# Performance work log

Hardware: AMD Instinct MI355X
Metric: run time of the kernel (lower is better)

## Reference

```python
import jax, jax.numpy as jnp
import numpy as np

B, A, H1, H2 = 128, 64, 256, 256


def setup_inputs() -> dict:
    key = jax.random.key(0)
    k1, k2, k3, k4, k5, k6 = jax.random.split(key, 6)
    scale = 0.01
    return {
        "userAspRep": jax.random.normal(k1, (B, A, H1), dtype=jnp.float32),
        "itemAspRep": jax.random.normal(k2, (B, A, H1), dtype=jnp.float32),
        "W_u": jax.random.uniform(k3, (H2, H1), jnp.float32, -scale, scale),
        "W_i": jax.random.uniform(k4, (H2, H1), jnp.float32, -scale, scale),
        "w_hu": jax.random.uniform(k5, (H2, 1), jnp.float32, -scale, scale),
        "w_hi": jax.random.uniform(k6, (H2, 1), jnp.float32, -scale, scale),
    }


def reference(userAspRep, itemAspRep, W_u, W_i, w_hu, w_hi):
    # L1 pairwise similarity: sim[b,u,i] = 1 / (1 + sum_h |U[b,u,h] - I[b,i,h]|)
    diff = jnp.abs(userAspRep[:, :, None, :] - itemAspRep[:, None, :, :])  # [B,Au,Ai,H1]
    sim = 1.0 / (1.0 + diff.sum(axis=-1))  # [B,Au,Ai]

    Wu_u = jnp.einsum('kh,buh->bku', W_u, userAspRep)  # [B,H2,Au]
    Wi_i = jnp.einsum('kh,bih->bki', W_i, itemAspRep)  # [B,H2,Ai]

    # User aspect importance
    H_u = jax.nn.relu(Wu_u + jnp.einsum('bki,bui->bku', Wi_i, sim))  # [B,H2,Au]
    user_scores = jnp.einsum('k,bku->bu', w_hu[:, 0], H_u)  # [B,Au]
    userAspImpt = jax.nn.softmax(user_scores, axis=1)

    # Item aspect importance
    H_i = jax.nn.relu(Wi_i + jnp.einsum('bku,bui->bki', Wu_u, sim))  # [B,H2,Ai]
    item_scores = jnp.einsum('k,bki->bi', w_hi[:, 0], H_i)  # [B,Ai]
    itemAspImpt = jax.nn.softmax(item_scores, axis=1)

    return (userAspImpt, itemAspImpt)
```

## Files before the change

kernel.cpp:

```cpp
#include <hip/hip_runtime.h>

#define NB 128
#define NA 64
#define NH1 256
#define NH2 256

typedef __attribute__((ext_vector_type(8))) short bf16x8;
typedef __attribute__((ext_vector_type(4))) float f32x4;
typedef __attribute__((ext_vector_type(8))) unsigned short u16x8;
typedef __attribute__((ext_vector_type(4))) unsigned short u16x4;
typedef _Float16 f16x2 __attribute__((ext_vector_type(2)));

__device__ __forceinline__ unsigned short f2bf(float f) {
    union { float f; unsigned u; } v; v.f = f;
    unsigned r = v.u + 0x7FFFu + ((v.u >> 16) & 1u);
    return (unsigned short)(r >> 16);
}
__device__ __forceinline__ f16x2 habs2(f16x2 x) {
    union { f16x2 h; unsigned u; } v; v.h = x; v.u &= 0x7FFF7FFFu; return v.h;
}

#define XSWZ(row, cb) ((cb) ^ (((row) & 7) << 4))

#define SROW 264
__global__ __launch_bounds__(1024) void sim_kernel(
    const float* __restrict__ U, const float* __restrict__ I,
    const float* __restrict__ Wu, const float* __restrict__ Wi,
    unsigned short* __restrict__ Wub, unsigned short* __restrict__ Wib,
    unsigned short* __restrict__ SIM, unsigned short* __restrict__ SIMT)
{
    __shared__ __align__(16) _Float16 sh[96 * SROW];
    const int t = threadIdx.x, b = blockIdx.x, uh = blockIdx.y;

    if (t < 512) {
        const int bl = b * 2 + uh;
        const int e = bl * 512 + t;
        if (e < 65536) Wub[e] = f2bf(Wu[e]);
        else           Wib[e - 65536] = f2bf(Wi[e - 65536]);
    }

    const float4* Ug = reinterpret_cast<const float4*>(U + ((size_t)b * NA + uh * 32) * NH1);
    const float4* Ig = reinterpret_cast<const float4*>(I + (size_t)b * NA * NH1);
    #pragma unroll
    for (int it = 0; it < 6; ++it) {
        const int g = t + it * 1024;
        float4 v = (g < 2048) ? Ug[g] : Ig[g - 2048];
        const int row = g >> 6, c4 = g & 63;
        f16x2 h0; h0.x = (_Float16)v.x; h0.y = (_Float16)v.y;
        f16x2 h1; h1.x = (_Float16)v.z; h1.y = (_Float16)v.w;
        union { f16x2 h[2]; float2 f; } pk; pk.h[0] = h0; pk.h[1] = h1;
        *reinterpret_cast<float2*>(&sh[row * SROW + c4 * 4]) = pk.f;
    }
    __syncthreads();

    const int tx = t & 15;
    const int hh = (t >> 4) & 1;
    const int ty = t >> 5;
    f16x2 acc[4];
    #pragma unroll
    for (int di = 0; di < 4; ++di) { acc[di].x = (_Float16)0; acc[di].y = (_Float16)0; }

    const _Float16* Urow = &sh[ty * SROW + hh * 128];
    #pragma unroll 4
    for (int h8 = 0; h8 < 16; ++h8) {
        union { float4 f; f16x2 h[4]; } uv, iv;
        uv.f = *reinterpret_cast<const float4*>(&Urow[h8 * 8]);
        #pragma unroll
        for (int di = 0; di < 4; ++di) {
            iv.f = *reinterpret_cast<const float4*>(
                &sh[(32 + tx + di * 16) * SROW + hh * 128 + h8 * 8]);
            #pragma unroll
            for (int c = 0; c < 4; ++c)
                acc[di] = acc[di] + habs2(uv.h[c] - iv.h[c]);
        }
    }

    float s[4];
    #pragma unroll
    for (int di = 0; di < 4; ++di) {
        s[di] = (float)acc[di].x + (float)acc[di].y;
        s[di] += __shfl_xor(s[di], 16, 64);
    }
    if (hh == 0) {
        const int u = uh * 32 + ty;
        unsigned short* SB = SIM  + (size_t)b * NA * NA;
        unsigned short* TB = SIMT + (size_t)b * NA * NA;
        #pragma unroll
        for (int di = 0; di < 4; ++di) {
            const int i = tx + di * 16;
            const unsigned short sv = f2bf(1.0f / (1.0f + s[di]));
            SB[(size_t)u * NA + i] = sv;
            TB[(size_t)i * NA + u] = sv;
        }
    }
}

__global__ __launch_bounds__(1024) void fused_kernel(
    const float* __restrict__ U, const float* __restrict__ I,
    const unsigned short* __restrict__ Wub, const unsigned short* __restrict__ Wib,
    const unsigned short* __restrict__ SIM, const unsigned short* __restrict__ SIMT,
    const float* __restrict__ whu, const float* __restrict__ whi,
    float* __restrict__ out)
{
    __shared__ __align__(16) unsigned short Xl[2 * 64 * 256];
    __shared__ __align__(16) unsigned short Pl[256 * 64];
    __shared__ float red[16 * 64];
    const int t = threadIdx.x, b = blockIdx.x, s = blockIdx.y;

    #pragma unroll
    for (int it = 0; it < 8; ++it) {
        const int g = t + it * 1024;
        const int side = g >> 12, rem = g & 4095;
        const int row = rem >> 6, c4 = rem & 63;
        const float* X = side ? I : U;
        float4 v = *reinterpret_cast<const float4*>(X + ((size_t)b * NA + row) * NH1 + c4 * 4);
        u16x4 o;
        o[0] = f2bf(v.x); o[1] = f2bf(v.y); o[2] = f2bf(v.z); o[3] = f2bf(v.w);
        char* dst = (char*)Xl + side * 32768 + row * 512 + XSWZ(row, c4 * 8);
        *reinterpret_cast<u16x4*>(dst) = o;
    }
    __syncthreads();

    const int w  = __builtin_amdgcn_readfirstlane(t >> 6);
    const int l  = t & 63;
    const int lr = l & 15;
    const int lk = (l >> 4) * 8;
    const int k0 = w * 16;

    const unsigned short* Ws = s ? Wib : Wub;
    const unsigned short* Wo = s ? Wub : Wib;

    f32x4 accO[4], accX[4];
    #pragma unroll
    for (int at = 0; at < 4; ++at) { accO[at] = (f32x4)(0.f); accX[at] = (f32x4)(0.f); }

    #pragma unroll
    for (int h0 = 0; h0 < NH1; h0 += 32) {
        bf16x8 as_, ao_, bs_[4], bo_[4];
        const size_t roff = (size_t)(k0 + lr) * NH1 + h0 + lk;
        as_ = *reinterpret_cast<const bf16x8*>(Ws + roff);
        ao_ = *reinterpret_cast<const bf16x8*>(Wo + roff);
        #pragma unroll
        for (int at = 0; at < 4; ++at) {
            const int row = at * 16 + lr;
            const int cb  = XSWZ(row, (h0 + lk) * 2);
            bs_[at] = *reinterpret_cast<const bf16x8*>((char*)Xl + s * 32768 + row * 512 + cb);
            bo_[at] = *reinterpret_cast<const bf16x8*>((char*)Xl + (s ^ 1) * 32768 + row * 512 + cb);
        }
        #pragma unroll
        for (int at = 0; at < 4; ++at) {
            accO[at] = __builtin_amdgcn_mfma_f32_16x16x32_bf16(as_, bs_[at], accO[at], 0, 0, 0);
            accX[at] = __builtin_amdgcn_mfma_f32_16x16x32_bf16(ao_, bo_[at], accX[at], 0, 0, 0);
        }
    }

    {
        const int kb = k0 + (l >> 4) * 4;
        #pragma unroll
        for (int at = 0; at < 4; ++at)
            #pragma unroll
            for (int r = 0; r < 4; ++r) {
                const int row = kb + r;
                *reinterpret_cast<unsigned short*>(
                    (char*)Pl + row * 128 + XSWZ(row, (at * 16 + lr) * 2)) = f2bf(accX[at][r]);
            }
    }
    __syncthreads();

    const unsigned short* SMg = (s ? SIMT : SIM) + (size_t)b * NA * NA;
    const float* wv = s ? whi : whu;

    f32x4 sacc[4];
    #pragma unroll
    for (int ot = 0; ot < 4; ++ot) sacc[ot] = (f32x4)(0.f);
    #pragma unroll
    for (int kk2 = 0; kk2 < 2; ++kk2) {
        const int arow = k0 + lr;
        bf16x8 af = *reinterpret_cast<const bf16x8*>(
            (char*)Pl + arow * 128 + XSWZ(arow, (kk2 * 32 + lk) * 2));
        #pragma unroll
        for (int ot = 0; ot < 4; ++ot) {
            bf16x8 bf = *reinterpret_cast<const bf16x8*>(
                SMg + (size_t)(ot * 16 + lr) * NA + kk2 * 32 + lk);
            sacc[ot] = __builtin_amdgcn_mfma_f32_16x16x32_bf16(af, bf, sacc[ot], 0, 0, 0);
        }
    }

    const int kb = k0 + (l >> 4) * 4;
    float wr[4];
    #pragma unroll
    for (int r = 0; r < 4; ++r) wr[r] = wv[kb + r];
    float partial[4];
    #pragma unroll
    for (int ot = 0; ot < 4; ++ot) {
        float p = 0.f;
        #pragma unroll
        for (int r = 0; r < 4; ++r) {
            float h = accO[ot][r] + sacc[ot][r];
            h = fmaxf(h, 0.f);
            p = fmaf(wr[r], h, p);
        }
        partial[ot] = p;
    }
    #pragma unroll
    for (int ot = 0; ot < 4; ++ot) {
        partial[ot] += __shfl_xor(partial[ot], 16, 64);
        partial[ot] += __shfl_xor(partial[ot], 32, 64);
    }
    if (l < 16) {
        #pragma unroll
        for (int ot = 0; ot < 4; ++ot) red[w * 64 + ot * 16 + l] = partial[ot];
    }
    __syncthreads();

    if (t < 64) {
        float sc = 0.f;
        #pragma unroll
        for (int q = 0; q < 16; ++q) sc += red[q * 64 + t];
        float m = sc;
        #pragma unroll
        for (int off = 32; off >= 1; off >>= 1) m = fmaxf(m, __shfl_xor(m, off, 64));
        float e = __expf(sc - m);
        float ssum = e;
        #pragma unroll
        for (int off = 32; off >= 1; off >>= 1) ssum += __shfl_xor(ssum, off, 64);
        out[(size_t)s * (NB * NA) + (size_t)b * NA + t] = e / ssum;
    }
}

extern "C" void kernel_launch(void* const* d_in, const int* in_sizes, int n_in,
                              void* d_out, int out_size, void* d_ws, size_t ws_size,
                              hipStream_t stream)
{
    (void)in_sizes; (void)n_in; (void)out_size; (void)ws_size;
    const float* U   = (const float*)d_in[0];
    const float* I   = (const float*)d_in[1];
    const float* Wu  = (const float*)d_in[2];
    const float* Wi  = (const float*)d_in[3];
    const float* whu = (const float*)d_in[4];
    const float* whi = (const float*)d_in[5];
    float* out = (float*)d_out;

    char* ws = (char*)d_ws;
    unsigned short* Wub   = (unsigned short*)(ws);
    unsigned short* Wib   = (unsigned short*)(ws + 131072);
    unsigned short* SIMb  = (unsigned short*)(ws + 262144);
    unsigned short* SIMTb = (unsigned short*)(ws + 1310720);

    sim_kernel<<<dim3(NB, 2), 1024, 0, stream>>>(U, I, Wu, Wi, Wub, Wib, SIMb, SIMTb);
    fused_kernel<<<dim3(NB, 2), 1024, 0, stream>>>(U, I, Wub, Wib, SIMb, SIMTb, whu, whi, out);
}
```

Baseline: 97.86 us.

## Fuse similarity computation into single aspect kernel with fp16 MFMA

Merges the separate similarity kernel into the main kernel, so each block computes the full 64x64 L1 similarity matrix from the fp16 inputs already staged in LDS and keeps it in shared memory rather than writing it and its transpose to global memory. Weights are read as fp32 and converted to fp16 in registers, which removes the bf16 weight pre-pass and the workspace. All MMAs switch from bf16 to fp16. To overlap work, half the waves do the projection first and the other half do the similarity first. The cost is that each of the two side-blocks recomputes the same similarity matrix, and the weight conversion is repeated per block.

```diff
diff --git a/kernel.cpp b/kernel.cpp
--- a/kernel.cpp
+++ b/kernel.cpp
@@ -5,106 +5,27 @@
 #define NH1 256
 #define NH2 256
 
-typedef __attribute__((ext_vector_type(8))) short bf16x8;
 typedef __attribute__((ext_vector_type(4))) float f32x4;
-typedef __attribute__((ext_vector_type(8))) unsigned short u16x8;
-typedef __attribute__((ext_vector_type(4))) unsigned short u16x4;
+typedef _Float16 f16x8 __attribute__((ext_vector_type(8)));
 typedef _Float16 f16x2 __attribute__((ext_vector_type(2)));
 
-__device__ __forceinline__ unsigned short f2bf(float f) {
-    union { float f; unsigned u; } v; v.f = f;
-    unsigned r = v.u + 0x7FFFu + ((v.u >> 16) & 1u);
-    return (unsigned short)(r >> 16);
-}
 __device__ __forceinline__ f16x2 habs2(f16x2 x) {
     union { f16x2 h; unsigned u; } v; v.h = x; v.u &= 0x7FFF7FFFu; return v.h;
 }
 
 #define XSWZ(row, cb) ((cb) ^ (((row) & 7) << 4))
 
-#define SROW 264
-__global__ __launch_bounds__(1024) void sim_kernel(
+__global__ __launch_bounds__(1024) void aspect_kernel(
     const float* __restrict__ U, const float* __restrict__ I,
     const float* __restrict__ Wu, const float* __restrict__ Wi,
-    unsigned short* __restrict__ Wub, unsigned short* __restrict__ Wib,
-    unsigned short* __restrict__ SIM, unsigned short* __restrict__ SIMT)
-{
-    __shared__ __align__(16) _Float16 sh[96 * SROW];
-    const int t = threadIdx.x, b = blockIdx.x, uh = blockIdx.y;
-
-    if (t < 512) {
-        const int bl = b * 2 + uh;
-        const int e = bl * 512 + t;
-        if (e < 65536) Wub[e] = f2bf(Wu[e]);
-        else           Wib[e - 65536] = f2bf(Wi[e - 65536]);
-    }
-
-    const float4* Ug = reinterpret_cast<const float4*>(U + ((size_t)b * NA + uh * 32) * NH1);
-    const float4* Ig = reinterpret_cast<const float4*>(I + (size_t)b * NA * NH1);
-    #pragma unroll
-    for (int it = 0; it < 6; ++it) {
-        const int g = t + it * 1024;
-        float4 v = (g < 2048) ? Ug[g] : Ig[g - 2048];
-        const int row = g >> 6, c4 = g & 63;
-        f16x2 h0; h0.x = (_Float16)v.x; h0.y = (_Float16)v.y;
-        f16x2 h1; h1.x = (_Float16)v.z; h1.y = (_Float16)v.w;
-        union { f16x2 h[2]; float2 f; } pk; pk.h[0] = h0; pk.h[1] = h1;
-        *reinterpret_cast<float2*>(&sh[row * SROW + c4 * 4]) = pk.f;
-    }
-    __syncthreads();
-
-    const int tx = t & 15;
-    const int hh = (t >> 4) & 1;
-    const int ty = t >> 5;
-    f16x2 acc[4];
-    #pragma unroll
-    for (int di = 0; di < 4; ++di) { acc[di].x = (_Float16)0; acc[di].y = (_Float16)0; }
-
-    const _Float16* Urow = &sh[ty * SROW + hh * 128];
-    #pragma unroll 4
-    for (int h8 = 0; h8 < 16; ++h8) {
-        union { float4 f; f16x2 h[4]; } uv, iv;
-        uv.f = *reinterpret_cast<const float4*>(&Urow[h8 * 8]);
-        #pragma unroll
-        for (int di = 0; di < 4; ++di) {
-            iv.f = *reinterpret_cast<const float4*>(
-                &sh[(32 + tx + di * 16) * SROW + hh * 128 + h8 * 8]);
-            #pragma unroll
-            for (int c = 0; c < 4; ++c)
-                acc[di] = acc[di] + habs2(uv.h[c] - iv.h[c]);
-        }
-    }
-
-    float s[4];
-    #pragma unroll
-    for (int di = 0; di < 4; ++di) {
-        s[di] = (float)acc[di].x + (float)acc[di].y;
-        s[di] += __shfl_xor(s[di], 16, 64);
-    }
-    if (hh == 0) {
-        const int u = uh * 32 + ty;
-        unsigned short* SB = SIM  + (size_t)b * NA * NA;
-        unsigned short* TB = SIMT + (size_t)b * NA * NA;
-        #pragma unroll
-        for (int di = 0; di < 4; ++di) {
-            const int i = tx + di * 16;
-            const unsigned short sv = f2bf(1.0f / (1.0f + s[di]));
-            SB[(size_t)u * NA + i] = sv;
-            TB[(size_t)i * NA + u] = sv;
-        }
-    }
-}
-
-__global__ __launch_bounds__(1024) void fused_kernel(
-    const float* __restrict__ U, const float* __restrict__ I,
-    const unsigned short* __restrict__ Wub, const unsigned short* __restrict__ Wib,
-    const unsigned short* __restrict__ SIM, const unsigned short* __restrict__ SIMT,
     const float* __restrict__ whu, const float* __restrict__ whi,
     float* __restrict__ out)
 {
-    __shared__ __align__(16) unsigned short Xl[2 * 64 * 256];
-    __shared__ __align__(16) unsigned short Pl[256 * 64];
+    __shared__ __align__(16) _Float16 Xl[2 * 64 * 256];
+    __shared__ __align__(16) _Float16 Pl[256 * 64];
+    __shared__ __align__(16) _Float16 SMl[64 * 64];
     __shared__ float red[16 * 64];
+
     const int t = threadIdx.x, b = blockIdx.x, s = blockIdx.y;
 
     #pragma unroll
@@ -114,10 +35,10 @@
         const int row = rem >> 6, c4 = rem & 63;
         const float* X = side ? I : U;
         float4 v = *reinterpret_cast<const float4*>(X + ((size_t)b * NA + row) * NH1 + c4 * 4);
-        u16x4 o;
-        o[0] = f2bf(v.x); o[1] = f2bf(v.y); o[2] = f2bf(v.z); o[3] = f2bf(v.w);
-        char* dst = (char*)Xl + side * 32768 + row * 512 + XSWZ(row, c4 * 8);
-        *reinterpret_cast<u16x4*>(dst) = o;
+        union { f16x2 h[2]; float2 f; } pk;
+        pk.h[0][0] = (_Float16)v.x; pk.h[0][1] = (_Float16)v.y;
+        pk.h[1][0] = (_Float16)v.z; pk.h[1][1] = (_Float16)v.w;
+        *reinterpret_cast<float2*>((char*)Xl + side * 32768 + row * 512 + XSWZ(row, c4 * 8)) = pk.f;
     }
     __syncthreads();
 
@@ -127,76 +48,135 @@
     const int lk = (l >> 4) * 8;
     const int k0 = w * 16;
 
-    const unsigned short* Ws = s ? Wib : Wub;
-    const unsigned short* Wo = s ? Wub : Wib;
-
-    f32x4 accO[4], accX[4];
-    #pragma unroll
-    for (int at = 0; at < 4; ++at) { accO[at] = (f32x4)(0.f); accX[at] = (f32x4)(0.f); }
-
-    #pragma unroll
-    for (int h0 = 0; h0 < NH1; h0 += 32) {
-        bf16x8 as_, ao_, bs_[4], bo_[4];
-        const size_t roff = (size_t)(k0 + lr) * NH1 + h0 + lk;
-        as_ = *reinterpret_cast<const bf16x8*>(Ws + roff);
-        ao_ = *reinterpret_cast<const bf16x8*>(Wo + roff);
-        #pragma unroll
-        for (int at = 0; at < 4; ++at) {
-            const int row = at * 16 + lr;
-            const int cb  = XSWZ(row, (h0 + lk) * 2);
-            bs_[at] = *reinterpret_cast<const bf16x8*>((char*)Xl + s * 32768 + row * 512 + cb);
-            bo_[at] = *reinterpret_cast<const bf16x8*>((char*)Xl + (s ^ 1) * 32768 + row * 512 + cb);
-        }
-        #pragma unroll
-        for (int at = 0; at < 4; ++at) {
-            accO[at] = __builtin_amdgcn_mfma_f32_16x16x32_bf16(as_, bs_[at], accO[at], 0, 0, 0);
-            accX[at] = __builtin_amdgcn_mfma_f32_16x16x32_bf16(ao_, bo_[at], accX[at], 0, 0, 0);
-        }
-    }
-
-    {
-        const int kb = k0 + (l >> 4) * 4;
+    const float* Ws = s ? Wi : Wu;
+    const float* Wo = s ? Wu : Wi;
+
+    f32x4 accO[4];
+
+    auto proj_and_pl = [&]() {
+        f32x4 accX[4];
+        #pragma unroll
+        for (int at = 0; at < 4; ++at) { accO[at] = (f32x4)(0.f); accX[at] = (f32x4)(0.f); }
+        #pragma unroll
+        for (int h0 = 0; h0 < NH1; h0 += 32) {
+            const float* wsp = Ws + (size_t)(k0 + lr) * NH1 + h0 + lk;
+            const float* wop = Wo + (size_t)(k0 + lr) * NH1 + h0 + lk;
+            float4 wa = *reinterpret_cast<const float4*>(wsp);
+            float4 wb = *reinterpret_cast<const float4*>(wsp + 4);
+            float4 xa = *reinterpret_cast<const float4*>(wop);
+            float4 xb = *reinterpret_cast<const float4*>(wop + 4);
+            f16x8 as_, ao_;
+            as_[0]=(_Float16)wa.x; as_[1]=(_Float16)wa.y; as_[2]=(_Float16)wa.z; as_[3]=(_Float16)wa.w;
+            as_[4]=(_Float16)wb.x; as_[5]=(_Float16)wb.y; as_[6]=(_Float16)wb.z; as_[7]=(_Float16)wb.w;
+            ao_[0]=(_Float16)xa.x; ao_[1]=(_Float16)xa.y; ao_[2]=(_Float16)xa.z; ao_[3]=(_Float16)xa.w;
+            ao_[4]=(_Float16)xb.x; ao_[5]=(_Float16)xb.y; ao_[6]=(_Float16)xb.z; ao_[7]=(_Float16)xb.w;
+            f16x8 bs_[4], bo_[4];
+            #pragma unroll
+            for (int at = 0; at < 4; ++at) {
+                const int row = at * 16 + lr;
+                const int cb  = XSWZ(row, (h0 + lk) * 2);
+                bs_[at] = *reinterpret_cast<const f16x8*>((char*)Xl + s * 32768 + row * 512 + cb);
+                bo_[at] = *reinterpret_cast<const f16x8*>((char*)Xl + (s ^ 1) * 32768 + row * 512 + cb);
+            }
+            #pragma unroll
+            for (int at = 0; at < 4; ++at) {
+                accO[at] = __builtin_amdgcn_mfma_f32_16x16x32_f16(as_, bs_[at], accO[at], 0, 0, 0);
+                accX[at] = __builtin_amdgcn_mfma_f32_16x16x32_f16(ao_, bo_[at], accX[at], 0, 0, 0);
+            }
+        }
+        const int kb4 = k0 + (l >> 4) * 4;
         #pragma unroll
         for (int at = 0; at < 4; ++at)
             #pragma unroll
             for (int r = 0; r < 4; ++r) {
-                const int row = kb + r;
-                *reinterpret_cast<unsigned short*>(
-                    (char*)Pl + row * 128 + XSWZ(row, (at * 16 + lr) * 2)) = f2bf(accX[at][r]);
-            }
-    }
+                const int row = kb4 + r;
+                *reinterpret_cast<_Float16*>(
+                    (char*)Pl + row * 128 + XSWZ(row, (at * 16 + lr) * 2)) = (_Float16)accX[at][r];
+            }
+    };
+
+    const int tx = t & 15;
+    const int hh = (t >> 4) & 1;
+    const int ty = t >> 5;
+    auto sim_part = [&]() {
+        union F4 { float4 f; f16x2 h[4]; };
+        f16x2 sa[2][4];
+        #pragma unroll
+        for (int du = 0; du < 2; ++du)
+            #pragma unroll
+            for (int di = 0; di < 4; ++di) { sa[du][di][0] = (_Float16)0; sa[du][di][1] = (_Float16)0; }
+        const int hb = hh * 256;
+        #pragma unroll 4
+        for (int h8 = 0; h8 < 16; ++h8) {
+            const int cbb = hb + h8 * 16;
+            F4 uc[2], ic[4];
+            #pragma unroll
+            for (int du = 0; du < 2; ++du) {
+                const int row = ty + du * 32;
+                uc[du].f = *reinterpret_cast<const float4*>((char*)Xl + row * 512 + XSWZ(row, cbb));
+            }
+            #pragma unroll
+            for (int di = 0; di < 4; ++di) {
+                const int row = tx + di * 16;
+                ic[di].f = *reinterpret_cast<const float4*>((char*)Xl + 32768 + row * 512 + XSWZ(row, cbb));
+            }
+            #pragma unroll
+            for (int du = 0; du < 2; ++du)
+                #pragma unroll
+                for (int di = 0; di < 4; ++di)
+                    #pragma unroll
+                    for (int c = 0; c < 4; ++c)
+                        sa[du][di] = sa[du][di] + habs2(uc[du].h[c] - ic[di].h[c]);
+        }
+        #pragma unroll
+        for (int du = 0; du < 2; ++du)
+            #pragma unroll
+            for (int di = 0; di < 4; ++di) {
+                float sum = (float)sa[du][di][0] + (float)sa[du][di][1];
+                sum += __shfl_xor(sum, 16, 64);
+                if (hh == 0) {
+                    const int u = ty + du * 32, i = tx + di * 16;
+                    const int own = s ? i : u, oth = s ? u : i;
+                    *reinterpret_cast<_Float16*>(
+                        (char*)SMl + own * 128 + XSWZ(own, oth * 2)) =
+                        (_Float16)(1.0f / (1.0f + sum));
+                }
+            }
+    };
+
+    if (w < 8) { proj_and_pl(); sim_part(); }
+    else       { sim_part(); proj_and_pl(); }
     __syncthreads();
 
-    const unsigned short* SMg = (s ? SIMT : SIM) + (size_t)b * NA * NA;
     const float* wv = s ? whi : whu;
-
-    f32x4 sacc[4];
-    #pragma unroll
-    for (int ot = 0; ot < 4; ++ot) sacc[ot] = (f32x4)(0.f);
+    f32x4 sc4[4];
+    #pragma unroll
+    for (int ot = 0; ot < 4; ++ot) sc4[ot] = (f32x4)(0.f);
+    const int arow = k0 + lr;
     #pragma unroll
     for (int kk2 = 0; kk2 < 2; ++kk2) {
-        const int arow = k0 + lr;
-        bf16x8 af = *reinterpret_cast<const bf16x8*>(
+        f16x8 af = *reinterpret_cast<const f16x8*>(
             (char*)Pl + arow * 128 + XSWZ(arow, (kk2 * 32 + lk) * 2));
         #pragma unroll
         for (int ot = 0; ot < 4; ++ot) {
-            bf16x8 bf = *reinterpret_cast<const bf16x8*>(
-                SMg + (size_t)(ot * 16 + lr) * NA + kk2 * 32 + lk);
-            sacc[ot] = __builtin_amdgcn_mfma_f32_16x16x32_bf16(af, bf, sacc[ot], 0, 0, 0);
-        }
-    }
-
-    const int kb = k0 + (l >> 4) * 4;
+            const int srow = ot * 16 + lr;
+            f16x8 bf = *reinterpret_cast<const f16x8*>(
+                (char*)SMl + srow * 128 + XSWZ(srow, (kk2 * 32 + lk) * 2));
+            sc4[ot] = __builtin_amdgcn_mfma_f32_16x16x32_f16(af, bf, sc4[ot], 0, 0, 0);
+        }
+    }
+
+    const int kb4 = k0 + (l >> 4) * 4;
     float wr[4];
     #pragma unroll
-    for (int r = 0; r < 4; ++r) wr[r] = wv[kb + r];
+    for (int r = 0; r < 4; ++r) wr[r] = wv[kb4 + r];
     float partial[4];
     #pragma unroll
     for (int ot = 0; ot < 4; ++ot) {
         float p = 0.f;
         #pragma unroll
         for (int r = 0; r < 4; ++r) {
-            float h = accO[ot][r] + sacc[ot][r];
+            float h = accO[ot][r] + sc4[ot][r];
             h = fmaxf(h, 0.f);
             p = fmaf(wr[r], h, p);
         }
@@ -232,7 +212,7 @@
                               void* d_out, int out_size, void* d_ws, size_t ws_size,
                               hipStream_t stream)
 {
-    (void)in_sizes; (void)n_in; (void)out_size; (void)ws_size;
+    (void)in_sizes; (void)n_in; (void)out_size; (void)d_ws; (void)ws_size;
     const float* U   = (const float*)d_in[0];
     const float* I   = (const float*)d_in[1];
     const float* Wu  = (const float*)d_in[2];
@@ -241,12 +221,5 @@
     const float* whi = (const float*)d_in[5];
     float* out = (float*)d_out;
 
-    char* ws = (char*)d_ws;
-    unsigned short* Wub   = (unsigned short*)(ws);
-    unsigned short* Wib   = (unsigned short*)(ws + 131072);
-    unsigned short* SIMb  = (unsigned short*)(ws + 262144);
-    unsigned short* SIMTb = (unsigned short*)(ws + 1310720);
-
-    sim_kernel<<<dim3(NB, 2), 1024, 0, stream>>>(U, I, Wu, Wi, Wub, Wib, SIMb, SIMTb);
-    fused_kernel<<<dim3(NB, 2), 1024, 0, stream>>>(U, I, Wub, Wib, SIMb, SIMTb, whu, whi, out);
+    aspect_kernel<<<dim3(NB, 2), 1024, 0, stream>>>(U, I, Wu, Wi, whu, whi, out);
 }
```

New measurement: 92.98 us. 1.05x faster.
